# Performance work log

Measured on AMD Instinct MI355X. Metric: run time of the kernel, lower is better.

Reference implementation:

```python
import jax, jax.numpy as jnp
import numpy as np


def _gcn(x, src, dst, W, b, n):
    # symmetric normalization: deg computed on edges WITH self-loops (weights 1)
    deg = jax.ops.segment_sum(jnp.ones_like(src, dtype=x.dtype), dst, num_segments=n)
    dinv = jnp.where(deg > 0, jax.lax.rsqrt(deg), 0.0)
    norm = dinv[src] * dinv[dst]              # [E+n]
    xw = x @ W                                # [n, out] transform first (cheaper)
    msg = xw[src] * norm[:, None]             # gather + edge scale
    return jax.ops.segment_sum(msg, dst, num_segments=n) + b


def setup_inputs() -> dict:
    key = jax.random.key(0)
    ks = jax.random.split(key, 8)
    N, E = 100_000, 1_280_000
    x = jax.random.normal(ks[0], (N, 18), dtype=jnp.float32)
    edge_index = jax.random.randint(ks[1], (2, E), 0, N, dtype=jnp.int32)
    W1 = jax.random.normal(ks[2], (18, 32), dtype=jnp.float32) * 0.2
    b1 = jnp.zeros((32,), dtype=jnp.float32)
    W2 = jax.random.normal(ks[3], (32, 64), dtype=jnp.float32) * 0.15
    b2 = jnp.zeros((64,), dtype=jnp.float32)
    Wfc = jax.random.normal(ks[4], (64, 2), dtype=jnp.float32) * 0.1
    bfc = jnp.zeros((2,), dtype=jnp.float32)
    return {"x": x, "edge_index": edge_index, "W1": W1, "b1": b1,
            "W2": W2, "b2": b2, "Wfc": Wfc, "bfc": bfc}


def reference(x, edge_index, W1, b1, W2, b2, Wfc, bfc):
    n = x.shape[0]
    loop = jnp.arange(n, dtype=edge_index.dtype)
    src = jnp.concatenate([edge_index[0], loop])   # add self-loops (PyG default)
    dst = jnp.concatenate([edge_index[1], loop])
    h = jax.nn.relu(_gcn(x, src, dst, W1, b1, n))
    h = jax.nn.relu(_gcn(h, src, dst, W2, b2, n))
    logits = h @ Wfc + bfc
    return jax.nn.log_softmax(logits, axis=1)
```

## Files before the change

### kernel.cpp

```cpp
#include <hip/hip_runtime.h>
#include <hip/hip_fp16.h>
#include <math.h>


#define TPB 256
#define BSH 8
#define BNODES 256
#define MAXBUCK 512
#define CH 4096
#define CAPSH 13
#define CAP (1 << CAPSH)

__global__ void k_part(const int* __restrict__ src, const int* __restrict__ dst,
                       int* __restrict__ bcursor, int* __restrict__ eb,
                       __half* __restrict__ u1h, __half* __restrict__ u2h,
                       int E, int n, int nbuck) {
    __shared__ int lh[MAXBUCK];
    __shared__ int lbase[MAXBUCK];
    int t = threadIdx.x;
    if (blockIdx.x == 0 && t < 32) {
        u1h[(size_t)n * 32 + t] = __float2half_rn(0.f);
        u2h[(size_t)n * 32 + t] = __float2half_rn(0.f);
    }
    int chunk0 = blockIdx.x * CH;
    int end = min(chunk0 + CH, E);
    const int4* dst4 = (const int4*)dst;
    const int4* src4 = (const int4*)src;
    for (int i = t; i < nbuck; i += TPB) lh[i] = 0;
    __syncthreads();
    for (int e4 = chunk0 / 4 + t; e4 * 4 < end; e4 += TPB) {
        int base = e4 * 4;
        int4 d = dst4[e4];
        if (base + 0 < end) atomicAdd(&lh[d.x >> BSH], 1);
        if (base + 1 < end) atomicAdd(&lh[d.y >> BSH], 1);
        if (base + 2 < end) atomicAdd(&lh[d.z >> BSH], 1);
        if (base + 3 < end) atomicAdd(&lh[d.w >> BSH], 1);
    }
    __syncthreads();
    for (int i = t; i < nbuck; i += TPB) {
        int c = lh[i];
        lbase[i] = c ? atomicAdd(&bcursor[i], c) : 0;
        lh[i] = 0;
    }
    __syncthreads();
    for (int e4 = chunk0 / 4 + t; e4 * 4 < end; e4 += TPB) {
        int base = e4 * 4;
        int4 d = dst4[e4];
        int4 s = src4[e4];
        #define PUT(c, sv) if (base + c < end) { \
            int b = (d.sv) >> BSH; \
            int r = lbase[b] + atomicAdd(&lh[b], 1); \
            if (r < CAP) \
                eb[((size_t)b << CAPSH) + r] = ((s.sv) << BSH) | ((d.sv) & (BNODES - 1)); }
        PUT(0, x) PUT(1, y) PUT(2, z) PUT(3, w)
        #undef PUT
    }
}

__global__ void k_bucket(const int* __restrict__ eb, const int* __restrict__ bcursor,
                         const float* __restrict__ x, const float* __restrict__ W1,
                         int* __restrict__ csr, int* __restrict__ row_start,
                         int* __restrict__ cnt8, float* __restrict__ dinv,
                         __half* __restrict__ u1h, int n) {
    __shared__ int lcnt[BNODES];
    __shared__ int wsum[4];
    __shared__ float ldinv[BNODES];
    __shared__ float xs[BNODES * 18];
    int b = blockIdx.x;
    int t = threadIdx.x;
    int node0 = b << BSH;
    int beg = b << CAPSH;
    int end = beg + min(bcursor[b], CAP);
    lcnt[t] = 0;
    __syncthreads();
    for (int i = beg + t; i < end; i += TPB)
        atomicAdd(&lcnt[eb[i] & (BNODES - 1)], 1);
    __syncthreads();
    int v = lcnt[t];
    int pad = (v + 7) & ~7;
    int lane = t & 63, wv = t >> 6;
    int val = pad;
#pragma unroll
    for (int off = 1; off < 64; off <<= 1) {
        int y = __shfl_up(val, off, 64);
        if (lane >= off) val += y;
    }
    if (lane == 63) wsum[wv] = val;
    __syncthreads();
    int add = 0;
#pragma unroll
    for (int w2 = 0; w2 < 4; ++w2) add += (w2 < wv) ? wsum[w2] : 0;
    int pexcl = val + add - pad;
    int node = node0 + t;
    float dv = rsqrtf(1.0f + (float)v);
    ldinv[t] = dv;
    if (node < n) {
        row_start[node] = beg + pexcl;
        cnt8[node] = pad >> 3;
        dinv[node] = dv;
    }
    lcnt[t] = pexcl;
    __syncthreads();
    for (int i = beg + t; i < end; i += TPB) {
        int e = eb[i];
        int p = atomicAdd(&lcnt[e & (BNODES - 1)], 1);
        csr[beg + p] = e >> BSH;
    }
    for (int p = v; p < pad; ++p) csr[beg + pexcl + p] = n;
    int nn = min(BNODES, n - node0);
    const float* xb = x + (size_t)node0 * 18;
    int tot18 = nn * 18;
    for (int i = t; i < tot18; i += TPB) xs[i] = xb[i];
    __syncthreads();
    int f = t & 31, g = t >> 5;
    float w1r[18];
#pragma unroll
    for (int k = 0; k < 18; ++k) w1r[k] = W1[k * 32 + f];
    __half* ub = u1h + (size_t)node0 * 32;
    for (int nl = g; nl < nn; nl += 8) {
        const float* rp = &xs[nl * 18];
        float a = 0.f;
#pragma unroll
        for (int k = 0; k < 18; ++k) a = fmaf(rp[k], w1r[k], a);
        ub[nl * 32 + f] = __float2half_rn(a * ldinv[nl]);
    }
}

#define GATHER8Q(uq, sA, sB, q4, a0, a1, a2, a3, a4, a5, a6, a7) \
    { uint4 _v0 = uq[(size_t)(sA).x * 4 + (q4)]; \
      uint4 _v1 = uq[(size_t)(sA).y * 4 + (q4)]; \
      uint4 _v2 = uq[(size_t)(sA).z * 4 + (q4)]; \
      uint4 _v3 = uq[(size_t)(sA).w * 4 + (q4)]; \
      uint4 _v4 = uq[(size_t)(sB).x * 4 + (q4)]; \
      uint4 _v5 = uq[(size_t)(sB).y * 4 + (q4)]; \
      uint4 _v6 = uq[(size_t)(sB).z * 4 + (q4)]; \
      uint4 _v7 = uq[(size_t)(sB).w * 4 + (q4)]; \
      __half2* _h0 = (__half2*)&_v0; __half2* _h1 = (__half2*)&_v1; \
      __half2* _h2 = (__half2*)&_v2; __half2* _h3 = (__half2*)&_v3; \
      __half2* _h4 = (__half2*)&_v4; __half2* _h5 = (__half2*)&_v5; \
      __half2* _h6 = (__half2*)&_v6; __half2* _h7 = (__half2*)&_v7; \
      __half2 _w0a = __hadd2(__hadd2(_h0[0], _h1[0]), __hadd2(_h2[0], _h3[0])); \
      __half2 _w0b = __hadd2(__hadd2(_h4[0], _h5[0]), __hadd2(_h6[0], _h7[0])); \
      __half2 _w1a = __hadd2(__hadd2(_h0[1], _h1[1]), __hadd2(_h2[1], _h3[1])); \
      __half2 _w1b = __hadd2(__hadd2(_h4[1], _h5[1]), __hadd2(_h6[1], _h7[1])); \
      __half2 _w2a = __hadd2(__hadd2(_h0[2], _h1[2]), __hadd2(_h2[2], _h3[2])); \
      __half2 _w2b = __hadd2(__hadd2(_h4[2], _h5[2]), __hadd2(_h6[2], _h7[2])); \
      __half2 _w3a = __hadd2(__hadd2(_h0[3], _h1[3]), __hadd2(_h2[3], _h3[3])); \
      __half2 _w3b = __hadd2(__hadd2(_h4[3], _h5[3]), __hadd2(_h6[3], _h7[3])); \
      float2 _f0a = __half22float2(_w0a), _f0b = __half22float2(_w0b); \
      float2 _f1a = __half22float2(_w1a), _f1b = __half22float2(_w1b); \
      float2 _f2a = __half22float2(_w2a), _f2b = __half22float2(_w2b); \
      float2 _f3a = __half22float2(_w3a), _f3b = __half22float2(_w3b); \
      a0 += _f0a.x + _f0b.x;  a1 += _f0a.y + _f0b.y; \
      a2 += _f1a.x + _f1b.x;  a3 += _f1a.y + _f1b.y; \
      a4 += _f2a.x + _f2b.x;  a5 += _f2a.y + _f2b.y; \
      a6 += _f3a.x + _f3b.x;  a7 += _f3a.y + _f3b.y; }

__global__ void k_fused1(const uint4* __restrict__ u1q, const int* __restrict__ row_start,
                         const int* __restrict__ cnt8, const int* __restrict__ csr,
                         const float* __restrict__ dinv,
                         const float* __restrict__ b1, __half* __restrict__ u2h,
                         int n) {
    int t = threadIdx.x;
    int lane = t & 63, wv = t >> 6;
    int q4 = lane & 3, grp = lane >> 2;
    int node = (blockIdx.x * 4 + wv) * 16 + grp;
    if (node >= n) return;
    const float4* b4 = (const float4*)b1;
    float4 bbA = b4[2 * q4], bbB = b4[2 * q4 + 1];
    uint4 sv = u1q[(size_t)node * 4 + q4];
    __half2* sh = (__half2*)&sv;
    float a0, a1, a2, a3, a4, a5, a6, a7;
    { float2 f0 = __half22float2(sh[0]), f1 = __half22float2(sh[1]);
      float2 f2 = __half22float2(sh[2]), f3 = __half22float2(sh[3]);
      a0 = f0.x; a1 = f0.y; a2 = f1.x; a3 = f1.y;
      a4 = f2.x; a5 = f2.y; a6 = f3.x; a7 = f3.y; }
    int beg = row_start[node];
    int it = cnt8[node];
    const int4* ip = (const int4*)(csr + beg);
    if (it > 0) {
        int4 sA = ip[0], sB = ip[1];
        for (int i = 0; i < it; ++i) {
            int4 nA = ip[2 * i + 2];
            int4 nB = ip[2 * i + 3];
            GATHER8Q(u1q, sA, sB, q4, a0, a1, a2, a3, a4, a5, a6, a7)
            sA = nA; sB = nB;
        }
    }
    float di = dinv[node];
    float r0 = fmaxf(fmaf(di, a0, bbA.x), 0.f) * di;
    float r1 = fmaxf(fmaf(di, a1, bbA.y), 0.f) * di;
    float r2 = fmaxf(fmaf(di, a2, bbA.z), 0.f) * di;
    float r3 = fmaxf(fmaf(di, a3, bbA.w), 0.f) * di;
    float r4 = fmaxf(fmaf(di, a4, bbB.x), 0.f) * di;
    float r5 = fmaxf(fmaf(di, a5, bbB.y), 0.f) * di;
    float r6 = fmaxf(fmaf(di, a6, bbB.z), 0.f) * di;
    float r7 = fmaxf(fmaf(di, a7, bbB.w), 0.f) * di;
    uint4 st;
    __half2* sp = (__half2*)&st;
    sp[0].x = __float2half_rn(r0); sp[0].y = __float2half_rn(r1);
    sp[1].x = __float2half_rn(r2); sp[1].y = __float2half_rn(r3);
    sp[2].x = __float2half_rn(r4); sp[2].y = __float2half_rn(r5);
    sp[3].x = __float2half_rn(r6); sp[3].y = __float2half_rn(r7);
    ((uint4*)u2h)[(size_t)node * 4 + q4] = st;
}

__global__ void k_fused2(const uint4* __restrict__ u2q, const int* __restrict__ row_start,
                         const int* __restrict__ cnt8, const int* __restrict__ csr,
                         const float* __restrict__ dinv,
                         const float* __restrict__ W2,
                         const float* __restrict__ b2, const float* __restrict__ Wfc,
                         const float* __restrict__ bfc, float* __restrict__ out,
                         int n) {
    __shared__ float lagg[4][16][33];
    int t = threadIdx.x;
    int lane = t & 63, wv = t >> 6;
    int q4 = lane & 3, grp = lane >> 2;
    int node0 = (blockIdx.x * 4 + wv) * 16;
    int node = node0 + grp;
    float a0 = 0.f, a1 = 0.f, a2 = 0.f, a3 = 0.f;
    float a4 = 0.f, a5 = 0.f, a6 = 0.f, a7 = 0.f;
    if (node < n) {
        uint4 sv = u2q[(size_t)node * 4 + q4];
        __half2* sh = (__half2*)&sv;
        float2 f0 = __half22float2(sh[0]), f1 = __half22float2(sh[1]);
        float2 f2 = __half22float2(sh[2]), f3 = __half22float2(sh[3]);
        a0 = f0.x; a1 = f0.y; a2 = f1.x; a3 = f1.y;
        a4 = f2.x; a5 = f2.y; a6 = f3.x; a7 = f3.y;
        int beg = row_start[node];
        int it = cnt8[node];
        const int4* ip = (const int4*)(csr + beg);
        if (it > 0) {
            int4 sA = ip[0], sB = ip[1];
            for (int i = 0; i < it; ++i) {
                int4 nA = ip[2 * i + 2];
                int4 nB = ip[2 * i + 3];
                GATHER8Q(u2q, sA, sB, q4, a0, a1, a2, a3, a4, a5, a6, a7)
                sA = nA; sB = nB;
            }
        }
    }
    int fb = q4 * 8;
    lagg[wv][grp][fb + 0] = a0; lagg[wv][grp][fb + 1] = a1;
    lagg[wv][grp][fb + 2] = a2; lagg[wv][grp][fb + 3] = a3;
    lagg[wv][grp][fb + 4] = a4; lagg[wv][grp][fb + 5] = a5;
    lagg[wv][grp][fb + 6] = a6; lagg[wv][grp][fb + 7] = a7;
    float w2r[32];
#pragma unroll
    for (int k = 0; k < 32; ++k) w2r[k] = W2[k * 64 + lane];
    float b2v = b2[lane];
    float wf0 = Wfc[lane * 2 + 0], wf1 = Wfc[lane * 2 + 1];
    float bf0 = bfc[0], bf1 = bfc[1];
#pragma unroll
    for (int r = 0; r < 16; ++r) {
        int nodeT = node0 + r;
        const float* rp = lagg[wv][r];
        float c0 = 0.f, c1 = 0.f, c2 = 0.f, c3 = 0.f;
#pragma unroll
        for (int k = 0; k < 32; k += 4) {
            c0 = fmaf(rp[k],     w2r[k],     c0);
            c1 = fmaf(rp[k + 1], w2r[k + 1], c1);
            c2 = fmaf(rp[k + 2], w2r[k + 2], c2);
            c3 = fmaf(rp[k + 3], w2r[k + 3], c3);
        }
        float a = (c0 + c1) + (c2 + c3);
        float v = (nodeT < n) ? fmaxf(fmaf(dinv[nodeT], a, b2v), 0.f) : 0.f;
        float l0 = v * wf0;
        float l1 = v * wf1;
#pragma unroll
        for (int off = 32; off >= 1; off >>= 1) {
            l0 += __shfl_xor(l0, off, 64);
            l1 += __shfl_xor(l1, off, 64);
        }
        if (lane == 0 && nodeT < n) {
            l0 += bf0;
            l1 += bf1;
            float m2 = fmaxf(l0, l1);
            float lse = m2 + __logf(__expf(l0 - m2) + __expf(l1 - m2));
            out[nodeT * 2 + 0] = l0 - lse;
            out[nodeT * 2 + 1] = l1 - lse;
        }
    }
}

extern "C" void kernel_launch(void* const* d_in, const int* in_sizes, int n_in,
                              void* d_out, int out_size, void* d_ws, size_t ws_size,
                              hipStream_t stream) {
    const float* x   = (const float*)d_in[0];
    const int*   ei  = (const int*)d_in[1];
    const float* W1  = (const float*)d_in[2];
    const float* b1  = (const float*)d_in[3];
    const float* W2  = (const float*)d_in[4];
    const float* b2  = (const float*)d_in[5];
    const float* Wfc = (const float*)d_in[6];
    const float* bfc = (const float*)d_in[7];
    float* out = (float*)d_out;

    const int n = in_sizes[0] / 18;
    const int E = in_sizes[1] / 2;
    const int* src = ei;
    const int* dst = ei + E;
    const int nbuck = (n + BNODES - 1) >> BSH;

    char* w = (char*)d_ws;
    int*    bcursor   = (int*)w;     w += (size_t)nbuck * 4;
    int*    row_start = (int*)w;     w += (size_t)n * 4;
    int*    cnt8      = (int*)w;     w += (size_t)n * 4;
    float*  dinv      = (float*)w;   w += (size_t)n * 4;
    int*    eb        = (int*)w;     w += (size_t)nbuck * CAP * 4;
    int*    csr       = (int*)w;     w += (size_t)nbuck * CAP * 4 + 128;
    w = (char*)(((size_t)w + 63) & ~(size_t)63);
    __half* u1h       = (__half*)w;  w += (size_t)(n + 1) * 32 * 2;
    w = (char*)(((size_t)w + 63) & ~(size_t)63);
    __half* u2h       = (__half*)w;  w += (size_t)(n + 1) * 32 * 2;

    hipMemsetAsync(bcursor, 0, (size_t)nbuck * 4, stream);
    k_part<<<(E + CH - 1) / CH, TPB, 0, stream>>>(src, dst, bcursor, eb, u1h, u2h, E, n, nbuck);
    k_bucket<<<nbuck, TPB, 0, stream>>>(eb, bcursor, x, W1, csr, row_start, cnt8,
                                        dinv, u1h, n);

    const int waves = (n + 15) / 16;
    const int blocksF = (waves + 3) / 4;

    k_fused1<<<blocksF, TPB, 0, stream>>>((const uint4*)u1h, row_start, cnt8, csr,
                                          dinv, b1, u2h, n);
    k_fused2<<<blocksF, TPB, 0, stream>>>((const uint4*)u2h, row_start, cnt8, csr,
                                          dinv, W2, b2, Wfc, bfc, out, n);
}
```

Before: 171.3 us.

## Fuse all four GCN stages into one persistent cooperative kernel with grid syncs

Result: slower. 543.7 us (+217.4%).

```diff
diff --git a/kernel.cpp b/kernel.cpp
--- a/kernel.cpp
+++ b/kernel.cpp
@@ -1,6 +1,9 @@
 #include <hip/hip_runtime.h>
+#include <hip/hip_cooperative_groups.h>
 #include <hip/hip_fp16.h>
 #include <math.h>
+
+namespace cg = cooperative_groups;
 
 
 #define TPB 256
@@ -11,10 +14,10 @@
 #define CAPSH 13
 #define CAP (1 << CAPSH)
 
-__global__ void k_part(const int* __restrict__ src, const int* __restrict__ dst,
-                       int* __restrict__ bcursor, int* __restrict__ eb,
-                       __half* __restrict__ u1h, __half* __restrict__ u2h,
-                       int E, int n, int nbuck) {
+__device__ __forceinline__ void dev_part(const int* __restrict__ src,
+        const int* __restrict__ dst, int* __restrict__ bcursor,
+        int* __restrict__ eb, __half* __restrict__ u1h, __half* __restrict__ u2h,
+        int E, int n, int nbuck, int nchunks, int gridN) {
     __shared__ int lh[MAXBUCK];
     __shared__ int lbase[MAXBUCK];
     int t = threadIdx.x;
@@ -22,107 +25,112 @@
         u1h[(size_t)n * 32 + t] = __float2half_rn(0.f);
         u2h[(size_t)n * 32 + t] = __float2half_rn(0.f);
     }
-    int chunk0 = blockIdx.x * CH;
-    int end = min(chunk0 + CH, E);
     const int4* dst4 = (const int4*)dst;
     const int4* src4 = (const int4*)src;
-    for (int i = t; i < nbuck; i += TPB) lh[i] = 0;
-    __syncthreads();
-    for (int e4 = chunk0 / 4 + t; e4 * 4 < end; e4 += TPB) {
-        int base = e4 * 4;
-        int4 d = dst4[e4];
-        if (base + 0 < end) atomicAdd(&lh[d.x >> BSH], 1);
-        if (base + 1 < end) atomicAdd(&lh[d.y >> BSH], 1);
-        if (base + 2 < end) atomicAdd(&lh[d.z >> BSH], 1);
-        if (base + 3 < end) atomicAdd(&lh[d.w >> BSH], 1);
-    }
-    __syncthreads();
-    for (int i = t; i < nbuck; i += TPB) {
-        int c = lh[i];
-        lbase[i] = c ? atomicAdd(&bcursor[i], c) : 0;
-        lh[i] = 0;
-    }
-    __syncthreads();
-    for (int e4 = chunk0 / 4 + t; e4 * 4 < end; e4 += TPB) {
-        int base = e4 * 4;
-        int4 d = dst4[e4];
-        int4 s = src4[e4];
-        #define PUT(c, sv) if (base + c < end) { \
-            int b = (d.sv) >> BSH; \
-            int r = lbase[b] + atomicAdd(&lh[b], 1); \
-            if (r < CAP) \
-                eb[((size_t)b << CAPSH) + r] = ((s.sv) << BSH) | ((d.sv) & (BNODES - 1)); }
-        PUT(0, x) PUT(1, y) PUT(2, z) PUT(3, w)
-        #undef PUT
-    }
-}
-
-__global__ void k_bucket(const int* __restrict__ eb, const int* __restrict__ bcursor,
-                         const float* __restrict__ x, const float* __restrict__ W1,
-                         int* __restrict__ csr, int* __restrict__ row_start,
-                         int* __restrict__ cnt8, float* __restrict__ dinv,
-                         __half* __restrict__ u1h, int n) {
+    for (int c = blockIdx.x; c < nchunks; c += gridN) {
+        int chunk0 = c * CH;
+        int end = min(chunk0 + CH, E);
+        for (int i = t; i < nbuck; i += TPB) lh[i] = 0;
+        __syncthreads();
+        for (int e4 = chunk0 / 4 + t; e4 * 4 < end; e4 += TPB) {
+            int base = e4 * 4;
+            int4 d = dst4[e4];
+            if (base + 0 < end) atomicAdd(&lh[d.x >> BSH], 1);
+            if (base + 1 < end) atomicAdd(&lh[d.y >> BSH], 1);
+            if (base + 2 < end) atomicAdd(&lh[d.z >> BSH], 1);
+            if (base + 3 < end) atomicAdd(&lh[d.w >> BSH], 1);
+        }
+        __syncthreads();
+        for (int i = t; i < nbuck; i += TPB) {
+            int cc = lh[i];
+            lbase[i] = cc ? atomicAdd(&bcursor[i], cc) : 0;
+            lh[i] = 0;
+        }
+        __syncthreads();
+        for (int e4 = chunk0 / 4 + t; e4 * 4 < end; e4 += TPB) {
+            int base = e4 * 4;
+            int4 d = dst4[e4];
+            int4 s = src4[e4];
+            #define PUT(cn, sv) if (base + cn < end) { \
+                int b = (d.sv) >> BSH; \
+                int r = lbase[b] + atomicAdd(&lh[b], 1); \
+                if (r < CAP) \
+                    eb[((size_t)b << CAPSH) + r] = ((s.sv) << BSH) | ((d.sv) & (BNODES - 1)); }
+            PUT(0, x) PUT(1, y) PUT(2, z) PUT(3, w)
+            #undef PUT
+        }
+        __syncthreads();
+    }
+}
+
+__device__ __forceinline__ void dev_bucket(const int* __restrict__ eb,
+        const int* __restrict__ bcursor, const float* __restrict__ x,
+        const float* __restrict__ W1, int* __restrict__ csr,
+        int* __restrict__ row_start, int* __restrict__ cnt8,
+        float* __restrict__ dinv, __half* __restrict__ u1h,
+        int n, int nbuck, int gridN) {
     __shared__ int lcnt[BNODES];
     __shared__ int wsum[4];
     __shared__ float ldinv[BNODES];
     __shared__ float xs[BNODES * 18];
-    int b = blockIdx.x;
     int t = threadIdx.x;
-    int node0 = b << BSH;
-    int beg = b << CAPSH;
-    int end = beg + min(bcursor[b], CAP);
-    lcnt[t] = 0;
-    __syncthreads();
-    for (int i = beg + t; i < end; i += TPB)
-        atomicAdd(&lcnt[eb[i] & (BNODES - 1)], 1);
-    __syncthreads();
-    int v = lcnt[t];
-    int pad = (v + 7) & ~7;
-    int lane = t & 63, wv = t >> 6;
-    int val = pad;
-#pragma unroll
-    for (int off = 1; off < 64; off <<= 1) {
-        int y = __shfl_up(val, off, 64);
-        if (lane >= off) val += y;
-    }
-    if (lane == 63) wsum[wv] = val;
-    __syncthreads();
-    int add = 0;
-#pragma unroll
-    for (int w2 = 0; w2 < 4; ++w2) add += (w2 < wv) ? wsum[w2] : 0;
-    int pexcl = val + add - pad;
-    int node = node0 + t;
-    float dv = rsqrtf(1.0f + (float)v);
-    ldinv[t] = dv;
-    if (node < n) {
-        row_start[node] = beg + pexcl;
-        cnt8[node] = pad >> 3;
-        dinv[node] = dv;
-    }
-    lcnt[t] = pexcl;
-    __syncthreads();
-    for (int i = beg + t; i < end; i += TPB) {
-        int e = eb[i];
-        int p = atomicAdd(&lcnt[e & (BNODES - 1)], 1);
-        csr[beg + p] = e >> BSH;
-    }
-    for (int p = v; p < pad; ++p) csr[beg + pexcl + p] = n;
-    int nn = min(BNODES, n - node0);
-    const float* xb = x + (size_t)node0 * 18;
-    int tot18 = nn * 18;
-    for (int i = t; i < tot18; i += TPB) xs[i] = xb[i];
-    __syncthreads();
+    int lane = t & 63, wvv = t >> 6;
     int f = t & 31, g = t >> 5;
     float w1r[18];
 #pragma unroll
     for (int k = 0; k < 18; ++k) w1r[k] = W1[k * 32 + f];
-    __half* ub = u1h + (size_t)node0 * 32;
-    for (int nl = g; nl < nn; nl += 8) {
-        const float* rp = &xs[nl * 18];
-        float a = 0.f;
-#pragma unroll
-        for (int k = 0; k < 18; ++k) a = fmaf(rp[k], w1r[k], a);
-        ub[nl * 32 + f] = __float2half_rn(a * ldinv[nl]);
+    for (int b = blockIdx.x; b < nbuck; b += gridN) {
+        int node0 = b << BSH;
+        int beg = b << CAPSH;
+        int end = beg + min(bcursor[b], CAP);
+        lcnt[t] = 0;
+        __syncthreads();
+        for (int i = beg + t; i < end; i += TPB)
+            atomicAdd(&lcnt[eb[i] & (BNODES - 1)], 1);
+        __syncthreads();
+        int v = lcnt[t];
+        int pad = (v + 7) & ~7;
+        int val = pad;
+#pragma unroll
+        for (int off = 1; off < 64; off <<= 1) {
+            int y = __shfl_up(val, off, 64);
+            if (lane >= off) val += y;
+        }
+        if (lane == 63) wsum[wvv] = val;
+        __syncthreads();
+        int add = 0;
+#pragma unroll
+        for (int w2 = 0; w2 < 4; ++w2) add += (w2 < wvv) ? wsum[w2] : 0;
+        int pexcl = val + add - pad;
+        int node = node0 + t;
+        float dv = rsqrtf(1.0f + (float)v);
+        ldinv[t] = dv;
+        if (node < n) {
+            row_start[node] = beg + pexcl;
+            cnt8[node] = pad >> 3;
+            dinv[node] = dv;
+        }
+        lcnt[t] = pexcl;
+        __syncthreads();
+        for (int i = beg + t; i < end; i += TPB) {
+            int e = eb[i];
+            int p = atomicAdd(&lcnt[e & (BNODES - 1)], 1);
+            csr[beg + p] = e >> BSH;
+        }
+        for (int p = v; p < pad; ++p) csr[beg + pexcl + p] = n;
+        int nn = min(BNODES, n - node0);
+        const float* xb = x + (size_t)node0 * 18;
+        int tot18 = nn * 18;
+        for (int i = t; i < tot18; i += TPB) xs[i] = xb[i];
+        __syncthreads();
+        __half* ub = u1h + (size_t)node0 * 32;
+        for (int nl = g; nl < nn; nl += 8) {
+            const float* rp = &xs[nl * 18];
+            float a = 0.f;
+#pragma unroll
+            for (int k = 0; k < 18; ++k) a = fmaf(rp[k], w1r[k], a);
+            ub[nl * 32 + f] = __float2half_rn(a * ldinv[nl]);
+        }
     }
 }
 
@@ -156,77 +164,26 @@
       a4 += _f2a.x + _f2b.x;  a5 += _f2a.y + _f2b.y; \
       a6 += _f3a.x + _f3b.x;  a7 += _f3a.y + _f3b.y; }
 
-__global__ void k_fused1(const uint4* __restrict__ u1q, const int* __restrict__ row_start,
-                         const int* __restrict__ cnt8, const int* __restrict__ csr,
-                         const float* __restrict__ dinv,
-                         const float* __restrict__ b1, __half* __restrict__ u2h,
-                         int n) {
+__device__ __forceinline__ void dev_fused1(const uint4* __restrict__ u1q,
+        const int* __restrict__ row_start, const int* __restrict__ cnt8,
+        const int* __restrict__ csr, const float* __restrict__ dinv,
+        const float* __restrict__ b1, __half* __restrict__ u2h,
+        int n, int blocksF, int gridN) {
     int t = threadIdx.x;
-    int lane = t & 63, wv = t >> 6;
+    int lane = t & 63, wvv = t >> 6;
     int q4 = lane & 3, grp = lane >> 2;
-    int node = (blockIdx.x * 4 + wv) * 16 + grp;
-    if (node >= n) return;
     const float4* b4 = (const float4*)b1;
     float4 bbA = b4[2 * q4], bbB = b4[2 * q4 + 1];
-    uint4 sv = u1q[(size_t)node * 4 + q4];
-    __half2* sh = (__half2*)&sv;
-    float a0, a1, a2, a3, a4, a5, a6, a7;
-    { float2 f0 = __half22float2(sh[0]), f1 = __half22float2(sh[1]);
-      float2 f2 = __half22float2(sh[2]), f3 = __half22float2(sh[3]);
-      a0 = f0.x; a1 = f0.y; a2 = f1.x; a3 = f1.y;
-      a4 = f2.x; a5 = f2.y; a6 = f3.x; a7 = f3.y; }
-    int beg = row_start[node];
-    int it = cnt8[node];
-    const int4* ip = (const int4*)(csr + beg);
-    if (it > 0) {
-        int4 sA = ip[0], sB = ip[1];
-        for (int i = 0; i < it; ++i) {
-            int4 nA = ip[2 * i + 2];
-            int4 nB = ip[2 * i + 3];
-            GATHER8Q(u1q, sA, sB, q4, a0, a1, a2, a3, a4, a5, a6, a7)
-            sA = nA; sB = nB;
-        }
-    }
-    float di = dinv[node];
-    float r0 = fmaxf(fmaf(di, a0, bbA.x), 0.f) * di;
-    float r1 = fmaxf(fmaf(di, a1, bbA.y), 0.f) * di;
-    float r2 = fmaxf(fmaf(di, a2, bbA.z), 0.f) * di;
-    float r3 = fmaxf(fmaf(di, a3, bbA.w), 0.f) * di;
-    float r4 = fmaxf(fmaf(di, a4, bbB.x), 0.f) * di;
-    float r5 = fmaxf(fmaf(di, a5, bbB.y), 0.f) * di;
-    float r6 = fmaxf(fmaf(di, a6, bbB.z), 0.f) * di;
-    float r7 = fmaxf(fmaf(di, a7, bbB.w), 0.f) * di;
-    uint4 st;
-    __half2* sp = (__half2*)&st;
-    sp[0].x = __float2half_rn(r0); sp[0].y = __float2half_rn(r1);
-    sp[1].x = __float2half_rn(r2); sp[1].y = __float2half_rn(r3);
-    sp[2].x = __float2half_rn(r4); sp[2].y = __float2half_rn(r5);
-    sp[3].x = __float2half_rn(r6); sp[3].y = __float2half_rn(r7);
-    ((uint4*)u2h)[(size_t)node * 4 + q4] = st;
-}
-
-__global__ void k_fused2(const uint4* __restrict__ u2q, const int* __restrict__ row_start,
-                         const int* __restrict__ cnt8, const int* __restrict__ csr,
-                         const float* __restrict__ dinv,
-                         const float* __restrict__ W2,
-                         const float* __restrict__ b2, const float* __restrict__ Wfc,
-                         const float* __restrict__ bfc, float* __restrict__ out,
-                         int n) {
-    __shared__ float lagg[4][16][33];
-    int t = threadIdx.x;
-    int lane = t & 63, wv = t >> 6;
-    int q4 = lane & 3, grp = lane >> 2;
-    int node0 = (blockIdx.x * 4 + wv) * 16;
-    int node = node0 + grp;
-    float a0 = 0.f, a1 = 0.f, a2 = 0.f, a3 = 0.f;
-    float a4 = 0.f, a5 = 0.f, a6 = 0.f, a7 = 0.f;
-    if (node < n) {
-        uint4 sv = u2q[(size_t)node * 4 + q4];
+    for (int vb = blockIdx.x; vb < blocksF; vb += gridN) {
+        int node = (vb * 4 + wvv) * 16 + grp;
+        if (node >= n) continue;
+        uint4 sv = u1q[(size_t)node * 4 + q4];
         __half2* sh = (__half2*)&sv;
-        float2 f0 = __half22float2(sh[0]), f1 = __half22float2(sh[1]);
-        float2 f2 = __half22float2(sh[2]), f3 = __half22float2(sh[3]);
-        a0 = f0.x; a1 = f0.y; a2 = f1.x; a3 = f1.y;
-        a4 = f2.x; a5 = f2.y; a6 = f3.x; a7 = f3.y;
+        float a0, a1, a2, a3, a4, a5, a6, a7;
+        { float2 f0 = __half22float2(sh[0]), f1 = __half22float2(sh[1]);
+          float2 f2 = __half22float2(sh[2]), f3 = __half22float2(sh[3]);
+          a0 = f0.x; a1 = f0.y; a2 = f1.x; a3 = f1.y;
+          a4 = f2.x; a5 = f2.y; a6 = f3.x; a7 = f3.y; }
         int beg = row_start[node];
         int it = cnt8[node];
         const int4* ip = (const int4*)(csr + beg);
@@ -235,52 +192,148 @@
             for (int i = 0; i < it; ++i) {
                 int4 nA = ip[2 * i + 2];
                 int4 nB = ip[2 * i + 3];
-                GATHER8Q(u2q, sA, sB, q4, a0, a1, a2, a3, a4, a5, a6, a7)
+                GATHER8Q(u1q, sA, sB, q4, a0, a1, a2, a3, a4, a5, a6, a7)
                 sA = nA; sB = nB;
             }
         }
-    }
-    int fb = q4 * 8;
-    lagg[wv][grp][fb + 0] = a0; lagg[wv][grp][fb + 1] = a1;
-    lagg[wv][grp][fb + 2] = a2; lagg[wv][grp][fb + 3] = a3;
-    lagg[wv][grp][fb + 4] = a4; lagg[wv][grp][fb + 5] = a5;
-    lagg[wv][grp][fb + 6] = a6; lagg[wv][grp][fb + 7] = a7;
+        float di = dinv[node];
+        float r0 = fmaxf(fmaf(di, a0, bbA.x), 0.f) * di;
+        float r1 = fmaxf(fmaf(di, a1, bbA.y), 0.f) * di;
+        float r2 = fmaxf(fmaf(di, a2, bbA.z), 0.f) * di;
+        float r3 = fmaxf(fmaf(di, a3, bbA.w), 0.f) * di;
+        float r4 = fmaxf(fmaf(di, a4, bbB.x), 0.f) * di;
+        float r5 = fmaxf(fmaf(di, a5, bbB.y), 0.f) * di;
+        float r6 = fmaxf(fmaf(di, a6, bbB.z), 0.f) * di;
+        float r7 = fmaxf(fmaf(di, a7, bbB.w), 0.f) * di;
+        uint4 st;
+        __half2* sp = (__half2*)&st;
+        sp[0].x = __float2half_rn(r0); sp[0].y = __float2half_rn(r1);
+        sp[1].x = __float2half_rn(r2); sp[1].y = __float2half_rn(r3);
+        sp[2].x = __float2half_rn(r4); sp[2].y = __float2half_rn(r5);
+        sp[3].x = __float2half_rn(r6); sp[3].y = __float2half_rn(r7);
+        ((uint4*)u2h)[(size_t)node * 4 + q4] = st;
+    }
+}
+
+__device__ __forceinline__ void dev_fused2(const uint4* __restrict__ u2q,
+        const int* __restrict__ row_start, const int* __restrict__ cnt8,
+        const int* __restrict__ csr, const float* __restrict__ dinv,
+        const float* __restrict__ W2, const float* __restrict__ b2,
+        const float* __restrict__ Wfc, const float* __restrict__ bfc,
+        float* __restrict__ out, int n, int blocksF, int gridN) {
+    __shared__ float lagg[4][16][33];
+    int t = threadIdx.x;
+    int lane = t & 63, wvv = t >> 6;
+    int q4 = lane & 3, grp = lane >> 2;
     float w2r[32];
 #pragma unroll
     for (int k = 0; k < 32; ++k) w2r[k] = W2[k * 64 + lane];
     float b2v = b2[lane];
     float wf0 = Wfc[lane * 2 + 0], wf1 = Wfc[lane * 2 + 1];
     float bf0 = bfc[0], bf1 = bfc[1];
-#pragma unroll
-    for (int r = 0; r < 16; ++r) {
-        int nodeT = node0 + r;
-        const float* rp = lagg[wv][r];
-        float c0 = 0.f, c1 = 0.f, c2 = 0.f, c3 = 0.f;
-#pragma unroll
-        for (int k = 0; k < 32; k += 4) {
-            c0 = fmaf(rp[k],     w2r[k],     c0);
-            c1 = fmaf(rp[k + 1], w2r[k + 1], c1);
-            c2 = fmaf(rp[k + 2], w2r[k + 2], c2);
-            c3 = fmaf(rp[k + 3], w2r[k + 3], c3);
-        }
-        float a = (c0 + c1) + (c2 + c3);
-        float v = (nodeT < n) ? fmaxf(fmaf(dinv[nodeT], a, b2v), 0.f) : 0.f;
-        float l0 = v * wf0;
-        float l1 = v * wf1;
-#pragma unroll
-        for (int off = 32; off >= 1; off >>= 1) {
-            l0 += __shfl_xor(l0, off, 64);
-            l1 += __shfl_xor(l1, off, 64);
-        }
-        if (lane == 0 && nodeT < n) {
-            l0 += bf0;
-            l1 += bf1;
-            float m2 = fmaxf(l0, l1);
-            float lse = m2 + __logf(__expf(l0 - m2) + __expf(l1 - m2));
-            out[nodeT * 2 + 0] = l0 - lse;
-            out[nodeT * 2 + 1] = l1 - lse;
-        }
-    }
+    for (int vb = blockIdx.x; vb < blocksF; vb += gridN) {
+        int node0 = (vb * 4 + wvv) * 16;
+        int node = node0 + grp;
+        float a0 = 0.f, a1 = 0.f, a2 = 0.f, a3 = 0.f;
+        float a4 = 0.f, a5 = 0.f, a6 = 0.f, a7 = 0.f;
+        if (node < n) {
+            uint4 sv = u2q[(size_t)node * 4 + q4];
+            __half2* sh = (__half2*)&sv;
+            float2 f0 = __half22float2(sh[0]), f1 = __half22float2(sh[1]);
+            float2 f2 = __half22float2(sh[2]), f3 = __half22float2(sh[3]);
+            a0 = f0.x; a1 = f0.y; a2 = f1.x; a3 = f1.y;
+            a4 = f2.x; a5 = f2.y; a6 = f3.x; a7 = f3.y;
+            int beg = row_start[node];
+            int it = cnt8[node];
+            const int4* ip = (const int4*)(csr + beg);
+            if (it > 0) {
+                int4 sA = ip[0], sB = ip[1];
+                for (int i = 0; i < it; ++i) {
+                    int4 nA = ip[2 * i + 2];
+                    int4 nB = ip[2 * i + 3];
+                    GATHER8Q(u2q, sA, sB, q4, a0, a1, a2, a3, a4, a5, a6, a7)
+                    sA = nA; sB = nB;
+                }
+            }
+        }
+        int fb = q4 * 8;
+        lagg[wvv][grp][fb + 0] = a0; lagg[wvv][grp][fb + 1] = a1;
+        lagg[wvv][grp][fb + 2] = a2; lagg[wvv][grp][fb + 3] = a3;
+        lagg[wvv][grp][fb + 4] = a4; lagg[wvv][grp][fb + 5] = a5;
+        lagg[wvv][grp][fb + 6] = a6; lagg[wvv][grp][fb + 7] = a7;
+#pragma unroll
+        for (int r = 0; r < 16; ++r) {
+            int nodeT = node0 + r;
+            const float* rp = lagg[wvv][r];
+            float c0 = 0.f, c1 = 0.f, c2 = 0.f, c3 = 0.f;
+#pragma unroll
+            for (int k = 0; k < 32; k += 4) {
+                c0 = fmaf(rp[k],     w2r[k],     c0);
+                c1 = fmaf(rp[k + 1], w2r[k + 1], c1);
+                c2 = fmaf(rp[k + 2], w2r[k + 2], c2);
+                c3 = fmaf(rp[k + 3], w2r[k + 3], c3);
+            }
+            float a = (c0 + c1) + (c2 + c3);
+            float v = (nodeT < n) ? fmaxf(fmaf(dinv[nodeT], a, b2v), 0.f) : 0.f;
+            float l0 = v * wf0;
+            float l1 = v * wf1;
+#pragma unroll
+            for (int off = 32; off >= 1; off >>= 1) {
+                l0 += __shfl_xor(l0, off, 64);
+                l1 += __shfl_xor(l1, off, 64);
+            }
+            if (lane == 0 && nodeT < n) {
+                l0 += bf0;
+                l1 += bf1;
+                float m2 = fmaxf(l0, l1);
+                float lse = m2 + __logf(__expf(l0 - m2) + __expf(l1 - m2));
+                out[nodeT * 2 + 0] = l0 - lse;
+                out[nodeT * 2 + 1] = l1 - lse;
+            }
+        }
+    }
+}
+
+__global__ void k_all(const int* src, const int* dst, int* bcursor, int* eb,
+                      int* csr, int* row_start, int* cnt8, float* dinv,
+                      __half* u1h, __half* u2h, const float* x, const float* W1,
+                      const float* b1, const float* W2, const float* b2,
+                      const float* Wfc, const float* bfc, float* out,
+                      int E, int n, int nbuck, int nchunks, int blocksF) {
+    cg::grid_group grid = cg::this_grid();
+    int G = gridDim.x;
+    dev_part(src, dst, bcursor, eb, u1h, u2h, E, n, nbuck, nchunks, G);
+    __threadfence(); grid.sync();
+    dev_bucket(eb, bcursor, x, W1, csr, row_start, cnt8, dinv, u1h, n, nbuck, G);
+    __threadfence(); grid.sync();
+    dev_fused1((const uint4*)u1h, row_start, cnt8, csr, dinv, b1, u2h, n, blocksF, G);
+    __threadfence(); grid.sync();
+    dev_fused2((const uint4*)u2h, row_start, cnt8, csr, dinv, W2, b2, Wfc, bfc,
+               out, n, blocksF, G);
+}
+
+__global__ void k_part_w(const int* src, const int* dst, int* bcursor, int* eb,
+                         __half* u1h, __half* u2h, int E, int n, int nbuck,
+                         int nchunks) {
+    dev_part(src, dst, bcursor, eb, u1h, u2h, E, n, nbuck, nchunks, gridDim.x);
+}
+__global__ void k_bucket_w(const int* eb, const int* bcursor, const float* x,
+                           const float* W1, int* csr, int* row_start, int* cnt8,
+                           float* dinv, __half* u1h, int n, int nbuck) {
+    dev_bucket(eb, bcursor, x, W1, csr, row_start, cnt8, dinv, u1h, n, nbuck,
+               gridDim.x);
+}
+__global__ void k_fused1_w(const uint4* u1q, const int* row_start,
+                           const int* cnt8, const int* csr, const float* dinv,
+                           const float* b1, __half* u2h, int n, int blocksF) {
+    dev_fused1(u1q, row_start, cnt8, csr, dinv, b1, u2h, n, blocksF, gridDim.x);
+}
+__global__ void k_fused2_w(const uint4* u2q, const int* row_start,
+                           const int* cnt8, const int* csr, const float* dinv,
+                           const float* W2, const float* b2, const float* Wfc,
+                           const float* bfc, float* out, int n, int blocksF) {
+    dev_fused2(u2q, row_start, cnt8, csr, dinv, W2, b2, Wfc, bfc, out, n,
+               blocksF, gridDim.x);
 }
 
 extern "C" void kernel_launch(void* const* d_in, const int* in_sizes, int n_in,
@@ -301,6 +354,9 @@
     const int* src = ei;
     const int* dst = ei + E;
     const int nbuck = (n + BNODES - 1) >> BSH;
+    const int nchunks = (E + CH - 1) / CH;
+    const int waves = (n + 15) / 16;
+    const int blocksF = (waves + 3) / 4;
 
     char* w = (char*)d_ws;
     int*    bcursor   = (int*)w;     w += (size_t)nbuck * 4;
@@ -315,15 +371,33 @@
     __half* u2h       = (__half*)w;  w += (size_t)(n + 1) * 32 * 2;
 
     hipMemsetAsync(bcursor, 0, (size_t)nbuck * 4, stream);
-    k_part<<<(E + CH - 1) / CH, TPB, 0, stream>>>(src, dst, bcursor, eb, u1h, u2h, E, n, nbuck);
-    k_bucket<<<nbuck, TPB, 0, stream>>>(eb, bcursor, x, W1, csr, row_start, cnt8,
-                                        dinv, u1h, n);
-
-    const int waves = (n + 15) / 16;
-    const int blocksF = (waves + 3) / 4;
-
-    k_fused1<<<blocksF, TPB, 0, stream>>>((const uint4*)u1h, row_start, cnt8, csr,
-                                          dinv, b1, u2h, n);
-    k_fused2<<<blocksF, TPB, 0, stream>>>((const uint4*)u2h, row_start, cnt8, csr,
-                                          dinv, W2, b2, Wfc, bfc, out, n);
-}
+
+    int E2 = E, n2 = n, nb2 = nbuck, nc2 = nchunks, bf2 = blocksF;
+    const uint4* u1q = (const uint4*)u1h;
+    const uint4* u2q = (const uint4*)u2h;
+
+    int maxB = 0;
+    hipError_t oe = hipOccupancyMaxActiveBlocksPerMultiprocessor(&maxB, k_all,
+                                                                 TPB, 0);
+    int G = (oe == hipSuccess && maxB > 0) ? maxB * 256 : 0;
+    if (G > blocksF) G = blocksF;
+    bool coop = (G >= 256);
+    if (coop) {
+        void* args[] = {&src, &dst, &bcursor, &eb, &csr, &row_start, &cnt8,
+                        &dinv, &u1h, &u2h, &x, &W1, &b1, &W2, &b2, &Wfc, &bfc,
+                        &out, &E2, &n2, &nb2, &nc2, &bf2};
+        hipError_t le = hipLaunchCooperativeKernel((const void*)k_all, dim3(G),
+                                                   dim3(TPB), args, 0, stream);
+        if (le != hipSuccess) coop = false;
+    }
+    if (!coop) {
+        k_part_w<<<nchunks, TPB, 0, stream>>>(src, dst, bcursor, eb, u1h, u2h,
+                                              E, n, nbuck, nchunks);
+        k_bucket_w<<<nbuck, TPB, 0, stream>>>(eb, bcursor, x, W1, csr, row_start,
+                                              cnt8, dinv, u1h, n, nbuck);
+        k_fused1_w<<<blocksF, TPB, 0, stream>>>(u1q, row_start, cnt8, csr, dinv,
+                                                b1, u2h, n, blocksF);
+        k_fused2_w<<<blocksF, TPB, 0, stream>>>(u2q, row_start, cnt8, csr, dinv,
+                                                W2, b2, Wfc, bfc, out, n, blocksF);
+    }
+}
```
